# Optimization experiments

Hardware: AMD Instinct MI355X
Metric: run time of the kernel (lower is better)

## Reference

```python
import jax, jax.numpy as jnp
import numpy as np

N_NODES = 100000
N_EDGES = 3200000
D_IN = 128
D_OUT = 128


def setup_inputs() -> dict:
    key = jax.random.key(0)
    k1, k2, k3 = jax.random.split(key, 3)
    x = jax.random.normal(k1, (N_NODES, D_IN), dtype=jnp.float32)
    edge_index = jax.random.randint(k2, (2, N_EDGES), 0, N_NODES, dtype=jnp.int64)
    # Glorot-style init for GCN weight
    W = jax.random.normal(k3, (D_IN, D_OUT), dtype=jnp.float32) * (1.0 / np.sqrt(D_IN))
    b = jnp.zeros((D_OUT,), dtype=jnp.float32)
    return {"x": x, "edge_index": edge_index, "W": W, "b": b}


def reference(x, edge_index, W, b):
    # GCNConv (PyG semantics): add self-loops, symmetric normalization
    # D^-1/2 A D^-1/2, linear transform, aggregate, add bias; then ReLU.
    N = x.shape[0]
    loops = jnp.arange(N, dtype=edge_index.dtype)
    row = jnp.concatenate([edge_index[0], loops])  # source nodes
    col = jnp.concatenate([edge_index[1], loops])  # target nodes
    # degree over targets, with self-loop weight 1
    deg = jax.ops.segment_sum(jnp.ones_like(col, dtype=x.dtype), col,
                              num_segments=N)
    dinv = jnp.where(deg > 0, 1.0 / jnp.sqrt(deg), 0.0)
    norm = dinv[row] * dinv[col]                   # [E+N]
    xl = x @ W                                     # [N, D_OUT] dense GEMM
    msgs = xl[row] * norm[:, None]                 # gather + scale  [E+N, D_OUT]
    agg = jax.ops.segment_sum(msgs, col, num_segments=N)  # scatter-add
    return jax.nn.relu(agg + b)
```

## Files before the change

### kernel.cpp

```cpp
#include <hip/hip_runtime.h>
#include <hip/hip_bf16.h>
#include <math.h>

#define DF 128
#define TILE_EDGES 6144
#define NPB 256
#define NB_MAX 512
#define KP 136

typedef __hip_bfloat16 bf16;
typedef __hip_bfloat162 bf16x2;
typedef __attribute__((ext_vector_type(8))) short short8;
typedef __attribute__((ext_vector_type(4))) float f32x4;

__device__ inline short bf16bits(float f) {
    __hip_bfloat16 h = __float2bfloat16(f);
    return *reinterpret_cast<short*>(&h);
}

__device__ inline float4 unpack4(float2 p) {
    unsigned u0 = __float_as_uint(p.x), u1 = __float_as_uint(p.y);
    float4 r;
    r.x = __uint_as_float(u0 << 16);
    r.y = __uint_as_float(u0 & 0xffff0000u);
    r.z = __uint_as_float(u1 << 16);
    r.w = __uint_as_float(u1 & 0xffff0000u);
    return r;
}

__global__ __launch_bounds__(512) void k_hist(const int* __restrict__ col,
                                              int* __restrict__ bucketCnt,
                                              int E, int NB) {
    __shared__ int h[NB_MAX];
    int tid = threadIdx.x;
    for (int i = tid; i < NB; i += 512) h[i] = 0;
    __syncthreads();
    for (int e = blockIdx.x * 512 + tid; e < E; e += gridDim.x * 512)
        atomicAdd(&h[col[e] >> 8], 1);
    __syncthreads();
    for (int i = tid; i < NB; i += 512)
        if (h[i]) atomicAdd(&bucketCnt[i], h[i]);
}

__global__ __launch_bounds__(512) void k_scanbkt(const int* __restrict__ bucketCnt,
                                                 int* __restrict__ bucketBase,
                                                 int* __restrict__ cursor,
                                                 int NB, int E) {
    __shared__ int tmp[512];
    int tid = threadIdx.x;
    int v = (tid < NB) ? bucketCnt[tid] : 0;
    tmp[tid] = v;
    __syncthreads();
    for (int off = 1; off < 512; off <<= 1) {
        int t = (tid >= off) ? tmp[tid - off] : 0;
        __syncthreads();
        tmp[tid] += t;
        __syncthreads();
    }
    if (tid < NB) {
        int excl = tmp[tid] - v;
        bucketBase[tid] = excl;
        cursor[tid] = excl;
    }
    if (tid == 0) bucketBase[NB] = E;
}

__global__ __launch_bounds__(512) void k_binscatter(const int* __restrict__ edge,
                                                    int* __restrict__ cursor,
                                                    unsigned* __restrict__ binned,
                                                    int E, int NB) {
    __shared__ int h[NB_MAX];
    __shared__ int curl[NB_MAX];
    int tid = threadIdx.x;
    int tileBase = blockIdx.x * TILE_EDGES;
    for (int i = tid; i < NB; i += 512) h[i] = 0;
    __syncthreads();
    for (int j = 0; j < TILE_EDGES / 512; ++j) {
        int e = tileBase + j * 512 + tid;
        if (e < E) atomicAdd(&h[edge[E + e] >> 8], 1);
    }
    __syncthreads();
    for (int i = tid; i < NB; i += 512)
        curl[i] = h[i] ? atomicAdd(&cursor[i], h[i]) : 0;
    __syncthreads();
    for (int j = 0; j < TILE_EDGES / 512; ++j) {
        int e = tileBase + j * 512 + tid;
        if (e < E) {
            int r = edge[e];
            int c = edge[E + e];
            int pos = atomicAdd(&curl[c >> 8], 1);
            binned[pos] = ((unsigned)(c & (NPB - 1)) << 24) | (unsigned)r;
        }
    }
}

__global__ __launch_bounds__(512) void k_bucket(const unsigned* __restrict__ binned,
                                                const int* __restrict__ bucketBase,
                                                int* __restrict__ ssrc,
                                                int* __restrict__ offsets,
                                                int* __restrict__ deg,
                                                float* __restrict__ dinv, int N) {
    __shared__ int h[NPB], sc[NPB], cur[NPB];
    int tid = threadIdx.x;
    int b = blockIdx.x;
    int base = bucketBase[b];
    int cnt = bucketBase[b + 1] - base;
    if (tid < NPB) h[tid] = 0;
    __syncthreads();
    for (int i = tid; i < cnt; i += 512)
        atomicAdd(&h[binned[base + i] >> 24], 1);
    __syncthreads();
    if (tid < NPB) sc[tid] = h[tid];
    __syncthreads();
    for (int off = 1; off < NPB; off <<= 1) {
        int tv = (tid >= off && tid < NPB) ? sc[tid - off] : 0;
        __syncthreads();
        if (tid < NPB) sc[tid] += tv;
        __syncthreads();
    }
    if (tid < NPB) {
        int excl = sc[tid] - h[tid];
        cur[tid] = base + excl;
        int node = b * NPB + tid;
        if (node < N) {
            offsets[node] = base + excl;
            deg[node] = h[tid];
            dinv[node] = rsqrtf((float)(h[tid] + 1));
        }
    }
    __syncthreads();
    for (int i = tid; i < cnt; i += 512) {
        unsigned v = binned[base + i];
        int pos = atomicAdd(&cur[v >> 24], 1);
        ssrc[pos] = (int)(v & 0xFFFFFFu);
    }
}

__global__ __launch_bounds__(256) void k_gemm(const float* __restrict__ x,
                                              const float* __restrict__ W,
                                              const float* __restrict__ dinv,
                                              bf16* __restrict__ y, int N) {
    __shared__ bf16 Wt[DF * KP];
    int tid = threadIdx.x;
    for (int i = tid; i < DF * (DF / 4); i += 256) {
        int k = i >> 5;
        int n4 = (i & 31) * 4;
        float4 w = *(const float4*)(W + k * DF + n4);
        Wt[(n4 + 0) * KP + k] = __float2bfloat16(w.x);
        Wt[(n4 + 1) * KP + k] = __float2bfloat16(w.y);
        Wt[(n4 + 2) * KP + k] = __float2bfloat16(w.z);
        Wt[(n4 + 3) * KP + k] = __float2bfloat16(w.w);
    }
    __syncthreads();

    const int wv = tid >> 6;
    const int lane = tid & 63;
    const int m16 = lane & 15;
    const int q = lane >> 4;
    const int rbase = blockIdx.x * 64 + wv * 16;
    const int arow = min(rbase + m16, N - 1);

    f32x4 acc[8];
#pragma unroll
    for (int nt = 0; nt < 8; ++nt) acc[nt] = (f32x4){0.f, 0.f, 0.f, 0.f};

#pragma unroll
    for (int kc = 0; kc < 4; ++kc) {
        int k0 = kc * 32 + q * 8;
        float4 xa = *(const float4*)(x + (size_t)arow * DF + k0);
        float4 xb = *(const float4*)(x + (size_t)arow * DF + k0 + 4);
        short8 a;
        a[0] = bf16bits(xa.x); a[1] = bf16bits(xa.y);
        a[2] = bf16bits(xa.z); a[3] = bf16bits(xa.w);
        a[4] = bf16bits(xb.x); a[5] = bf16bits(xb.y);
        a[6] = bf16bits(xb.z); a[7] = bf16bits(xb.w);
#pragma unroll
        for (int nt = 0; nt < 8; ++nt) {
            short8 b = *(const short8*)(Wt + (nt * 16 + m16) * KP + k0);
            acc[nt] = __builtin_amdgcn_mfma_f32_16x16x32_bf16(a, b, acc[nt], 0, 0, 0);
        }
    }

#pragma unroll
    for (int r = 0; r < 4; ++r) {
        int orow = rbase + q * 4 + r;
        if (orow < N) {
            float dv = dinv[orow];
#pragma unroll
            for (int nt = 0; nt < 8; ++nt) {
                y[(size_t)orow * DF + nt * 16 + m16] = __float2bfloat16(acc[nt][r] * dv);
            }
        }
    }
}

__global__ __launch_bounds__(256) void k_gather(const float* __restrict__ yf,
                                                const int* __restrict__ ssrc,
                                                const int* __restrict__ offsets,
                                                const int* __restrict__ deg,
                                                const float* __restrict__ dinv,
                                                const float* __restrict__ bvec,
                                                float* __restrict__ out, int N) {
    int wave = (blockIdx.x * 256 + threadIdx.x) >> 6;
    int lane = threadIdx.x & 63;
    if (wave >= N) return;
    int c = wave;
    int start = offsets[c];
    int d = deg[c];
    int half = lane >> 5;
    int l32 = lane & 31;

    float4 acc = make_float4(0.f, 0.f, 0.f, 0.f);
    if (half == 0) {
        float2 sv = *(const float2*)(yf + (size_t)c * 64 + l32 * 2);
        acc = unpack4(sv);
    }

    for (int base = 0; base < d; base += 64) {
        int nb = min(64, d - base);
        int idx = ssrc[start + base + min(lane, nb - 1)];
        int j = 0;
        for (; j + 16 <= nb; j += 16) {
            int ra0 = __shfl(idx, j + 0),  rb0 = __shfl(idx, j + 1);
            int ra1 = __shfl(idx, j + 2),  rb1 = __shfl(idx, j + 3);
            int ra2 = __shfl(idx, j + 4),  rb2 = __shfl(idx, j + 5);
            int ra3 = __shfl(idx, j + 6),  rb3 = __shfl(idx, j + 7);
            int ra4 = __shfl(idx, j + 8),  rb4 = __shfl(idx, j + 9);
            int ra5 = __shfl(idx, j + 10), rb5 = __shfl(idx, j + 11);
            int ra6 = __shfl(idx, j + 12), rb6 = __shfl(idx, j + 13);
            int ra7 = __shfl(idx, j + 14), rb7 = __shfl(idx, j + 15);
            int r0 = half ? rb0 : ra0;
            int r1 = half ? rb1 : ra1;
            int r2 = half ? rb2 : ra2;
            int r3 = half ? rb3 : ra3;
            int r4 = half ? rb4 : ra4;
            int r5 = half ? rb5 : ra5;
            int r6 = half ? rb6 : ra6;
            int r7 = half ? rb7 : ra7;
            float2 v0 = *(const float2*)(yf + (size_t)r0 * 64 + l32 * 2);
            float2 v1 = *(const float2*)(yf + (size_t)r1 * 64 + l32 * 2);
            float2 v2 = *(const float2*)(yf + (size_t)r2 * 64 + l32 * 2);
            float2 v3 = *(const float2*)(yf + (size_t)r3 * 64 + l32 * 2);
            float2 v4 = *(const float2*)(yf + (size_t)r4 * 64 + l32 * 2);
            float2 v5 = *(const float2*)(yf + (size_t)r5 * 64 + l32 * 2);
            float2 v6 = *(const float2*)(yf + (size_t)r6 * 64 + l32 * 2);
            float2 v7 = *(const float2*)(yf + (size_t)r7 * 64 + l32 * 2);
            float4 u0 = unpack4(v0), u1 = unpack4(v1), u2 = unpack4(v2), u3 = unpack4(v3);
            float4 u4 = unpack4(v4), u5 = unpack4(v5), u6 = unpack4(v6), u7 = unpack4(v7);
            acc.x += ((u0.x + u1.x) + (u2.x + u3.x)) + ((u4.x + u5.x) + (u6.x + u7.x));
            acc.y += ((u0.y + u1.y) + (u2.y + u3.y)) + ((u4.y + u5.y) + (u6.y + u7.y));
            acc.z += ((u0.z + u1.z) + (u2.z + u3.z)) + ((u4.z + u5.z) + (u6.z + u7.z));
            acc.w += ((u0.w + u1.w) + (u2.w + u3.w)) + ((u4.w + u5.w) + (u6.w + u7.w));
        }
        for (; j + 2 <= nb; j += 2) {
            int ra = __shfl(idx, j), rb = __shfl(idx, j + 1);
            int r = half ? rb : ra;
            float2 v = *(const float2*)(yf + (size_t)r * 64 + l32 * 2);
            float4 u = unpack4(v);
            acc.x += u.x; acc.y += u.y; acc.z += u.z; acc.w += u.w;
        }
        if (j < nb) {
            int r = __shfl(idx, j);
            if (half == 0) {
                float2 v = *(const float2*)(yf + (size_t)r * 64 + l32 * 2);
                float4 u = unpack4(v);
                acc.x += u.x; acc.y += u.y; acc.z += u.z; acc.w += u.w;
            }
        }
    }

    acc.x += __shfl_xor(acc.x, 32);
    acc.y += __shfl_xor(acc.y, 32);
    acc.z += __shfl_xor(acc.z, 32);
    acc.w += __shfl_xor(acc.w, 32);

    if (half == 0) {
        float dv = dinv[c];
        float4 bb = *(const float4*)(bvec + l32 * 4);
        float4 o;
        o.x = fmaxf(fmaf(dv, acc.x, bb.x), 0.0f);
        o.y = fmaxf(fmaf(dv, acc.y, bb.y), 0.0f);
        o.z = fmaxf(fmaf(dv, acc.z, bb.z), 0.0f);
        o.w = fmaxf(fmaf(dv, acc.w, bb.w), 0.0f);
        *(float4*)(out + (size_t)c * DF + l32 * 4) = o;
    }
}

extern "C" void kernel_launch(void* const* d_in, const int* in_sizes, int n_in,
                              void* d_out, int out_size, void* d_ws, size_t ws_size,
                              hipStream_t stream) {
    const float* x    = (const float*)d_in[0];
    const int*   edge = (const int*)d_in[1];
    const float* W    = (const float*)d_in[2];
    const float* b    = (const float*)d_in[3];
    float*       out  = (float*)d_out;

    const int N = in_sizes[0] / DF;
    const int E = in_sizes[1] / 2;

    const int T  = (E + TILE_EDGES - 1) / TILE_EDGES;
    const int NB = (N + NPB - 1) / NPB;

    bf16*     y          = (bf16*)d_ws;
    int*      deg        = (int*)(y + (size_t)N * DF);
    float*    dinv       = (float*)(deg + N);
    int*      offsets    = (int*)(dinv + N);
    int*      bucketBase = offsets + N;
    int*      cursor     = bucketBase + NB_MAX + 8;
    int*      bucketCnt  = cursor + NB_MAX + 8;
    unsigned* binned     = (unsigned*)(bucketCnt + NB_MAX + 8);
    int*      ssrc       = (int*)(binned + E);

    (void)hipMemsetAsync(bucketCnt, 0, (NB + 1) * sizeof(int), stream);
    k_hist<<<512, 512, 0, stream>>>(edge + E, bucketCnt, E, NB);
    k_scanbkt<<<1, 512, 0, stream>>>(bucketCnt, bucketBase, cursor, NB, E);
    k_binscatter<<<T, 512, 0, stream>>>(edge, cursor, binned, E, NB);
    k_bucket<<<NB, 512, 0, stream>>>(binned, bucketBase, ssrc, offsets, deg, dinv, N);
    k_gemm<<<(N + 63) / 64, 256, 0, stream>>>(x, W, dinv, y, N);
    k_gather<<<(N + 3) / 4, 256, 0, stream>>>((const float*)y, ssrc, offsets, deg, dinv, b, out, N);
}
```

Measured before the change: 337.2 us.

## Split feature dimension into two halves with separate gather passes for cache locality

The GEMM now writes its bf16 output as two planar halves of 64 features each. The gather kernel runs twice, once per half, so each pass touches a 12.8 MB working set that fits better in cache, and each lane loads 4 bytes instead of 8. The cost is that index loads, shuffles and offset reads are done twice, and each gather request is narrower (128 B per row segment).

```diff
diff --git a/kernel.cpp b/kernel.cpp
--- a/kernel.cpp
+++ b/kernel.cpp
@@ -18,13 +18,11 @@
     return *reinterpret_cast<short*>(&h);
 }
 
-__device__ inline float4 unpack4(float2 p) {
-    unsigned u0 = __float_as_uint(p.x), u1 = __float_as_uint(p.y);
-    float4 r;
-    r.x = __uint_as_float(u0 << 16);
-    r.y = __uint_as_float(u0 & 0xffff0000u);
-    r.z = __uint_as_float(u1 << 16);
-    r.w = __uint_as_float(u1 & 0xffff0000u);
+__device__ inline float2 unpack2(float p) {
+    unsigned u = __float_as_uint(p);
+    float2 r;
+    r.x = __uint_as_float(u << 16);
+    r.y = __uint_as_float(u & 0xffff0000u);
     return r;
 }
 
@@ -188,19 +186,21 @@
             float dv = dinv[orow];
 #pragma unroll
             for (int nt = 0; nt < 8; ++nt) {
-                y[(size_t)orow * DF + nt * 16 + m16] = __float2bfloat16(acc[nt][r] * dv);
+                bf16* yp = y + (size_t)(nt >> 2) * (size_t)N * 64;
+                yp[(size_t)orow * 64 + (nt & 3) * 16 + m16] = __float2bfloat16(acc[nt][r] * dv);
             }
         }
     }
 }
 
-__global__ __launch_bounds__(256) void k_gather(const float* __restrict__ yf,
+__global__ __launch_bounds__(256) void k_gather(const float* __restrict__ yp,
                                                 const int* __restrict__ ssrc,
                                                 const int* __restrict__ offsets,
                                                 const int* __restrict__ deg,
                                                 const float* __restrict__ dinv,
                                                 const float* __restrict__ bvec,
-                                                float* __restrict__ out, int N) {
+                                                float* __restrict__ outp,
+                                                int N) {
     int wave = (blockIdx.x * 256 + threadIdx.x) >> 6;
     int lane = threadIdx.x & 63;
     if (wave >= N) return;
@@ -210,79 +210,61 @@
     int half = lane >> 5;
     int l32 = lane & 31;
 
-    float4 acc = make_float4(0.f, 0.f, 0.f, 0.f);
-    if (half == 0) {
-        float2 sv = *(const float2*)(yf + (size_t)c * 64 + l32 * 2);
-        acc = unpack4(sv);
-    }
+    float2 acc = make_float2(0.f, 0.f);
+    if (half == 0) acc = unpack2(yp[(size_t)c * 32 + l32]);
 
     for (int base = 0; base < d; base += 64) {
         int nb = min(64, d - base);
         int idx = ssrc[start + base + min(lane, nb - 1)];
         int j = 0;
         for (; j + 16 <= nb; j += 16) {
-            int ra0 = __shfl(idx, j + 0),  rb0 = __shfl(idx, j + 1);
-            int ra1 = __shfl(idx, j + 2),  rb1 = __shfl(idx, j + 3);
-            int ra2 = __shfl(idx, j + 4),  rb2 = __shfl(idx, j + 5);
-            int ra3 = __shfl(idx, j + 6),  rb3 = __shfl(idx, j + 7);
-            int ra4 = __shfl(idx, j + 8),  rb4 = __shfl(idx, j + 9);
-            int ra5 = __shfl(idx, j + 10), rb5 = __shfl(idx, j + 11);
-            int ra6 = __shfl(idx, j + 12), rb6 = __shfl(idx, j + 13);
-            int ra7 = __shfl(idx, j + 14), rb7 = __shfl(idx, j + 15);
-            int r0 = half ? rb0 : ra0;
-            int r1 = half ? rb1 : ra1;
-            int r2 = half ? rb2 : ra2;
-            int r3 = half ? rb3 : ra3;
-            int r4 = half ? rb4 : ra4;
-            int r5 = half ? rb5 : ra5;
-            int r6 = half ? rb6 : ra6;
-            int r7 = half ? rb7 : ra7;
-            float2 v0 = *(const float2*)(yf + (size_t)r0 * 64 + l32 * 2);
-            float2 v1 = *(const float2*)(yf + (size_t)r1 * 64 + l32 * 2);
-            float2 v2 = *(const float2*)(yf + (size_t)r2 * 64 + l32 * 2);
-            float2 v3 = *(const float2*)(yf + (size_t)r3 * 64 + l32 * 2);
-            float2 v4 = *(const float2*)(yf + (size_t)r4 * 64 + l32 * 2);
-            float2 v5 = *(const float2*)(yf + (size_t)r5 * 64 + l32 * 2);
-            float2 v6 = *(const float2*)(yf + (size_t)r6 * 64 + l32 * 2);
-            float2 v7 = *(const float2*)(yf + (size_t)r7 * 64 + l32 * 2);
-            float4 u0 = unpack4(v0), u1 = unpack4(v1), u2 = unpack4(v2), u3 = unpack4(v3);
-            float4 u4 = unpack4(v4), u5 = unpack4(v5), u6 = unpack4(v6), u7 = unpack4(v7);
+            int r0 = __shfl(idx, j + 0 + half);
+            int r1 = __shfl(idx, j + 2 + half);
+            int r2 = __shfl(idx, j + 4 + half);
+            int r3 = __shfl(idx, j + 6 + half);
+            int r4 = __shfl(idx, j + 8 + half);
+            int r5 = __shfl(idx, j + 10 + half);
+            int r6 = __shfl(idx, j + 12 + half);
+            int r7 = __shfl(idx, j + 14 + half);
+            float v0 = yp[(size_t)r0 * 32 + l32];
+            float v1 = yp[(size_t)r1 * 32 + l32];
+            float v2 = yp[(size_t)r2 * 32 + l32];
+            float v3 = yp[(size_t)r3 * 32 + l32];
+            float v4 = yp[(size_t)r4 * 32 + l32];
+            float v5 = yp[(size_t)r5 * 32 + l32];
+            float v6 = yp[(size_t)r6 * 32 + l32];
+            float v7 = yp[(size_t)r7 * 32 + l32];
+            float2 u0 = unpack2(v0), u1 = unpack2(v1), u2 = unpack2(v2), u3 = unpack2(v3);
+            float2 u4 = unpack2(v4), u5 = unpack2(v5), u6 = unpack2(v6), u7 = unpack2(v7);
             acc.x += ((u0.x + u1.x) + (u2.x + u3.x)) + ((u4.x + u5.x) + (u6.x + u7.x));
             acc.y += ((u0.y + u1.y) + (u2.y + u3.y)) + ((u4.y + u5.y) + (u6.y + u7.y));
-            acc.z += ((u0.z + u1.z) + (u2.z + u3.z)) + ((u4.z + u5.z) + (u6.z + u7.z));
-            acc.w += ((u0.w + u1.w) + (u2.w + u3.w)) + ((u4.w + u5.w) + (u6.w + u7.w));
         }
         for (; j + 2 <= nb; j += 2) {
-            int ra = __shfl(idx, j), rb = __shfl(idx, j + 1);
-            int r = half ? rb : ra;
-            float2 v = *(const float2*)(yf + (size_t)r * 64 + l32 * 2);
-            float4 u = unpack4(v);
-            acc.x += u.x; acc.y += u.y; acc.z += u.z; acc.w += u.w;
+            int r = __shfl(idx, j + half);
+            float2 u = unpack2(yp[(size_t)r * 32 + l32]);
+            acc.x += u.x;
+            acc.y += u.y;
         }
         if (j < nb) {
             int r = __shfl(idx, j);
             if (half == 0) {
-                float2 v = *(const float2*)(yf + (size_t)r * 64 + l32 * 2);
-                float4 u = unpack4(v);
-                acc.x += u.x; acc.y += u.y; acc.z += u.z; acc.w += u.w;
+                float2 u = unpack2(yp[(size_t)r * 32 + l32]);
+                acc.x += u.x;
+                acc.y += u.y;
             }
         }
     }
 
     acc.x += __shfl_xor(acc.x, 32);
     acc.y += __shfl_xor(acc.y, 32);
-    acc.z += __shfl_xor(acc.z, 32);
-    acc.w += __shfl_xor(acc.w, 32);
 
     if (half == 0) {
         float dv = dinv[c];
-        float4 bb = *(const float4*)(bvec + l32 * 4);
-        float4 o;
+        float2 bb = *(const float2*)(bvec + l32 * 2);
+        float2 o;
         o.x = fmaxf(fmaf(dv, acc.x, bb.x), 0.0f);
         o.y = fmaxf(fmaf(dv, acc.y, bb.y), 0.0f);
-        o.z = fmaxf(fmaf(dv, acc.z, bb.z), 0.0f);
-        o.w = fmaxf(fmaf(dv, acc.w, bb.w), 0.0f);
-        *(float4*)(out + (size_t)c * DF + l32 * 4) = o;
+        *(float2*)(outp + (size_t)c * DF + l32 * 2) = o;
     }
 }
 
@@ -317,5 +299,8 @@
     k_binscatter<<<T, 512, 0, stream>>>(edge, cursor, binned, E, NB);
     k_bucket<<<NB, 512, 0, stream>>>(binned, bucketBase, ssrc, offsets, deg, dinv, N);
     k_gemm<<<(N + 63) / 64, 256, 0, stream>>>(x, W, dinv, y, N);
-    k_gather<<<(N + 3) / 4, 256, 0, stream>>>((const float*)y, ssrc, offsets, deg, dinv, b, out, N);
-}
+    k_gather<<<(N + 3) / 4, 256, 0, stream>>>((const float*)y, ssrc, offsets, deg, dinv,
+                                              b, out, N);
+    k_gather<<<(N + 3) / 4, 256, 0, stream>>>((const float*)(y + (size_t)N * 64), ssrc,
+                                              offsets, deg, dinv, b + 64, out + 64, N);
+}
```

Measured after the change: 350.2 us. 3.8% more time.

## Replace two-level bucketed CSR build with global atomic histogram and scatter

Applied to the files above, without the earlier changes.

Replaces the bucket-binning CSR construction (per-bucket histogram, bin scatter, per-bucket local sort) with a direct global per-node degree histogram built by global atomics, a three-pass prefix scan over all nodes, and a scatter that claims slots by global atomic cursor increments. This drops one full intermediate pass over the edges and the binned buffer, at the cost of 3.2M contended global atomics twice and a less local write pattern for ssrc. The gather kernel now derives degree from consecutive offsets and uses a single shuffle with a lane-dependent source instead of two shuffles and a select.

```diff
diff --git a/kernel.cpp b/kernel.cpp
--- a/kernel.cpp
+++ b/kernel.cpp
@@ -3,9 +3,6 @@
 #include <math.h>
 
 #define DF 128
-#define TILE_EDGES 6144
-#define NPB 256
-#define NB_MAX 512
 #define KP 136
 
 typedef __hip_bfloat16 bf16;
@@ -28,27 +25,35 @@
     return r;
 }
 
-__global__ __launch_bounds__(512) void k_hist(const int* __restrict__ col,
-                                              int* __restrict__ bucketCnt,
-                                              int E, int NB) {
-    __shared__ int h[NB_MAX];
+__global__ __launch_bounds__(512) void k_deghist(const int* __restrict__ col,
+                                                 int* __restrict__ deg, int E) {
+    for (int e = blockIdx.x * 512 + threadIdx.x; e < E; e += gridDim.x * 512)
+        atomicAdd(&deg[col[e]], 1);
+}
+
+__global__ __launch_bounds__(256) void k_scanA(const int* __restrict__ deg,
+                                               int* __restrict__ offs,
+                                               int* __restrict__ blockSums, int Nn) {
+    __shared__ int tmp[256];
     int tid = threadIdx.x;
-    for (int i = tid; i < NB; i += 512) h[i] = 0;
+    int n = blockIdx.x * 256 + tid;
+    int v = (n < Nn) ? deg[n] : 0;
+    tmp[tid] = v;
     __syncthreads();
-    for (int e = blockIdx.x * 512 + tid; e < E; e += gridDim.x * 512)
-        atomicAdd(&h[col[e] >> 8], 1);
-    __syncthreads();
-    for (int i = tid; i < NB; i += 512)
-        if (h[i]) atomicAdd(&bucketCnt[i], h[i]);
-}
-
-__global__ __launch_bounds__(512) void k_scanbkt(const int* __restrict__ bucketCnt,
-                                                 int* __restrict__ bucketBase,
-                                                 int* __restrict__ cursor,
-                                                 int NB, int E) {
+    for (int off = 1; off < 256; off <<= 1) {
+        int t = (tid >= off) ? tmp[tid - off] : 0;
+        __syncthreads();
+        tmp[tid] += t;
+        __syncthreads();
+    }
+    if (tid == 255) blockSums[blockIdx.x] = tmp[255];
+    if (n < Nn) offs[n] = tmp[tid] - v;
+}
+
+__global__ __launch_bounds__(512) void k_scanB(int* __restrict__ blockSums, int nb) {
     __shared__ int tmp[512];
     int tid = threadIdx.x;
-    int v = (tid < NB) ? bucketCnt[tid] : 0;
+    int v = (tid < nb) ? blockSums[tid] : 0;
     tmp[tid] = v;
     __syncthreads();
     for (int off = 1; off < 512; off <<= 1) {
@@ -57,82 +62,33 @@
         tmp[tid] += t;
         __syncthreads();
     }
-    if (tid < NB) {
-        int excl = tmp[tid] - v;
-        bucketBase[tid] = excl;
-        cursor[tid] = excl;
-    }
-    if (tid == 0) bucketBase[NB] = E;
-}
-
-__global__ __launch_bounds__(512) void k_binscatter(const int* __restrict__ edge,
-                                                    int* __restrict__ cursor,
-                                                    unsigned* __restrict__ binned,
-                                                    int E, int NB) {
-    __shared__ int h[NB_MAX];
-    __shared__ int curl[NB_MAX];
-    int tid = threadIdx.x;
-    int tileBase = blockIdx.x * TILE_EDGES;
-    for (int i = tid; i < NB; i += 512) h[i] = 0;
-    __syncthreads();
-    for (int j = 0; j < TILE_EDGES / 512; ++j) {
-        int e = tileBase + j * 512 + tid;
-        if (e < E) atomicAdd(&h[edge[E + e] >> 8], 1);
-    }
-    __syncthreads();
-    for (int i = tid; i < NB; i += 512)
-        curl[i] = h[i] ? atomicAdd(&cursor[i], h[i]) : 0;
-    __syncthreads();
-    for (int j = 0; j < TILE_EDGES / 512; ++j) {
-        int e = tileBase + j * 512 + tid;
-        if (e < E) {
-            int r = edge[e];
-            int c = edge[E + e];
-            int pos = atomicAdd(&curl[c >> 8], 1);
-            binned[pos] = ((unsigned)(c & (NPB - 1)) << 24) | (unsigned)r;
-        }
-    }
-}
-
-__global__ __launch_bounds__(512) void k_bucket(const unsigned* __restrict__ binned,
-                                                const int* __restrict__ bucketBase,
-                                                int* __restrict__ ssrc,
-                                                int* __restrict__ offsets,
-                                                int* __restrict__ deg,
-                                                float* __restrict__ dinv, int N) {
-    __shared__ int h[NPB], sc[NPB], cur[NPB];
-    int tid = threadIdx.x;
-    int b = blockIdx.x;
-    int base = bucketBase[b];
-    int cnt = bucketBase[b + 1] - base;
-    if (tid < NPB) h[tid] = 0;
-    __syncthreads();
-    for (int i = tid; i < cnt; i += 512)
-        atomicAdd(&h[binned[base + i] >> 24], 1);
-    __syncthreads();
-    if (tid < NPB) sc[tid] = h[tid];
-    __syncthreads();
-    for (int off = 1; off < NPB; off <<= 1) {
-        int tv = (tid >= off && tid < NPB) ? sc[tid - off] : 0;
-        __syncthreads();
-        if (tid < NPB) sc[tid] += tv;
-        __syncthreads();
-    }
-    if (tid < NPB) {
-        int excl = sc[tid] - h[tid];
-        cur[tid] = base + excl;
-        int node = b * NPB + tid;
-        if (node < N) {
-            offsets[node] = base + excl;
-            deg[node] = h[tid];
-            dinv[node] = rsqrtf((float)(h[tid] + 1));
-        }
-    }
-    __syncthreads();
-    for (int i = tid; i < cnt; i += 512) {
-        unsigned v = binned[base + i];
-        int pos = atomicAdd(&cur[v >> 24], 1);
-        ssrc[pos] = (int)(v & 0xFFFFFFu);
+    if (tid < nb) blockSums[tid] = tmp[tid] - v;
+}
+
+__global__ __launch_bounds__(256) void k_scanC(const int* __restrict__ deg,
+                                               int* __restrict__ offs,
+                                               const int* __restrict__ blockSums,
+                                               int* __restrict__ cursor,
+                                               float* __restrict__ dinv,
+                                               int Nn, int E) {
+    int n = blockIdx.x * 256 + threadIdx.x;
+    if (n < Nn) {
+        int v = offs[n] + blockSums[n >> 8];
+        offs[n] = v;
+        cursor[n] = v;
+        dinv[n] = rsqrtf((float)(deg[n] + 1));
+    }
+    if (n == Nn) offs[Nn] = E;
+}
+
+__global__ __launch_bounds__(512) void k_scatter(const int* __restrict__ edge,
+                                                 int* __restrict__ cursor,
+                                                 int* __restrict__ ssrc, int E) {
+    for (int e = blockIdx.x * 512 + threadIdx.x; e < E; e += gridDim.x * 512) {
+        int r = edge[e];
+        int c = edge[E + e];
+        int pos = atomicAdd(&cursor[c], 1);
+        ssrc[pos] = r;
     }
 }
 
@@ -197,7 +153,6 @@
 __global__ __launch_bounds__(256) void k_gather(const float* __restrict__ yf,
                                                 const int* __restrict__ ssrc,
                                                 const int* __restrict__ offsets,
-                                                const int* __restrict__ deg,
                                                 const float* __restrict__ dinv,
                                                 const float* __restrict__ bvec,
                                                 float* __restrict__ out, int N) {
@@ -206,7 +161,7 @@
     if (wave >= N) return;
     int c = wave;
     int start = offsets[c];
-    int d = deg[c];
+    int d = offsets[c + 1] - start;
     int half = lane >> 5;
     int l32 = lane & 31;
 
@@ -221,22 +176,14 @@
         int idx = ssrc[start + base + min(lane, nb - 1)];
         int j = 0;
         for (; j + 16 <= nb; j += 16) {
-            int ra0 = __shfl(idx, j + 0),  rb0 = __shfl(idx, j + 1);
-            int ra1 = __shfl(idx, j + 2),  rb1 = __shfl(idx, j + 3);
-            int ra2 = __shfl(idx, j + 4),  rb2 = __shfl(idx, j + 5);
-            int ra3 = __shfl(idx, j + 6),  rb3 = __shfl(idx, j + 7);
-            int ra4 = __shfl(idx, j + 8),  rb4 = __shfl(idx, j + 9);
-            int ra5 = __shfl(idx, j + 10), rb5 = __shfl(idx, j + 11);
-            int ra6 = __shfl(idx, j + 12), rb6 = __shfl(idx, j + 13);
-            int ra7 = __shfl(idx, j + 14), rb7 = __shfl(idx, j + 15);
-            int r0 = half ? rb0 : ra0;
-            int r1 = half ? rb1 : ra1;
-            int r2 = half ? rb2 : ra2;
-            int r3 = half ? rb3 : ra3;
-            int r4 = half ? rb4 : ra4;
-            int r5 = half ? rb5 : ra5;
-            int r6 = half ? rb6 : ra6;
-            int r7 = half ? rb7 : ra7;
+            int r0 = __shfl(idx, j + 0 + half);
+            int r1 = __shfl(idx, j + 2 + half);
+            int r2 = __shfl(idx, j + 4 + half);
+            int r3 = __shfl(idx, j + 6 + half);
+            int r4 = __shfl(idx, j + 8 + half);
+            int r5 = __shfl(idx, j + 10 + half);
+            int r6 = __shfl(idx, j + 12 + half);
+            int r7 = __shfl(idx, j + 14 + half);
             float2 v0 = *(const float2*)(yf + (size_t)r0 * 64 + l32 * 2);
             float2 v1 = *(const float2*)(yf + (size_t)r1 * 64 + l32 * 2);
             float2 v2 = *(const float2*)(yf + (size_t)r2 * 64 + l32 * 2);
@@ -253,8 +200,7 @@
             acc.w += ((u0.w + u1.w) + (u2.w + u3.w)) + ((u4.w + u5.w) + (u6.w + u7.w));
         }
         for (; j + 2 <= nb; j += 2) {
-            int ra = __shfl(idx, j), rb = __shfl(idx, j + 1);
-            int r = half ? rb : ra;
+            int r = __shfl(idx, j + half);
             float2 v = *(const float2*)(yf + (size_t)r * 64 + l32 * 2);
             float4 u = unpack4(v);
             acc.x += u.x; acc.y += u.y; acc.z += u.z; acc.w += u.w;
@@ -298,24 +244,22 @@
     const int N = in_sizes[0] / DF;
     const int E = in_sizes[1] / 2;
 
-    const int T  = (E + TILE_EDGES - 1) / TILE_EDGES;
-    const int NB = (N + NPB - 1) / NPB;
-
     bf16*     y          = (bf16*)d_ws;
     int*      deg        = (int*)(y + (size_t)N * DF);
     float*    dinv       = (float*)(deg + N);
     int*      offsets    = (int*)(dinv + N);
-    int*      bucketBase = offsets + N;
-    int*      cursor     = bucketBase + NB_MAX + 8;
-    int*      bucketCnt  = cursor + NB_MAX + 8;
-    unsigned* binned     = (unsigned*)(bucketCnt + NB_MAX + 8);
-    int*      ssrc       = (int*)(binned + E);
-
-    (void)hipMemsetAsync(bucketCnt, 0, (NB + 1) * sizeof(int), stream);
-    k_hist<<<512, 512, 0, stream>>>(edge + E, bucketCnt, E, NB);
-    k_scanbkt<<<1, 512, 0, stream>>>(bucketCnt, bucketBase, cursor, NB, E);
-    k_binscatter<<<T, 512, 0, stream>>>(edge, cursor, binned, E, NB);
-    k_bucket<<<NB, 512, 0, stream>>>(binned, bucketBase, ssrc, offsets, deg, dinv, N);
+    int*      cursor     = offsets + N + 8;
+    int*      blockSums  = cursor + N;
+    int*      ssrc       = blockSums + 512;
+
+    const int nbN = (N + 255) / 256;
+
+    (void)hipMemsetAsync(deg, 0, N * sizeof(int), stream);
+    k_deghist<<<2048, 512, 0, stream>>>(edge + E, deg, E);
+    k_scanA<<<nbN, 256, 0, stream>>>(deg, offsets, blockSums, N);
+    k_scanB<<<1, 512, 0, stream>>>(blockSums, nbN);
+    k_scanC<<<nbN + 1, 256, 0, stream>>>(deg, offsets, blockSums, cursor, dinv, N, E);
+    k_scatter<<<2048, 512, 0, stream>>>(edge, cursor, ssrc, E);
     k_gemm<<<(N + 63) / 64, 256, 0, stream>>>(x, W, dinv, y, N);
-    k_gather<<<(N + 3) / 4, 256, 0, stream>>>((const float*)y, ssrc, offsets, deg, dinv, b, out, N);
-}
+    k_gather<<<(N + 3) / 4, 256, 0, stream>>>((const float*)y, ssrc, offsets, dinv, b, out, N);
+}
```

Measured after the change: 651.5 us. +93.2%, slower.
